# Performance work log

Measured on AMD Instinct MI355X. Metric: run time of the kernel, lower is better.

## Reference

```python
import math
import jax, jax.numpy as jnp
import numpy as np

H, N, L, B = 768, 64, 2048, 4
DT_MIN, DT_MAX = 1e-3, 1e-1


def setup_inputs() -> dict:
    key = jax.random.key(0)
    ks = jax.random.split(key, 7)
    # s4d_lin eigenvalue init: Re(lambda) = -0.5, Im(lambda) = pi*n
    log_neg_real = jnp.full((H, N), math.log(0.5), dtype=jnp.float32)
    imag = math.pi * jnp.broadcast_to(jnp.arange(N, dtype=jnp.float32)[None, :], (H, N))
    B_re = jax.random.normal(ks[0], (H, N), dtype=jnp.float32) * 0.5
    B_im = jax.random.normal(ks[1], (H, N), dtype=jnp.float32) * 0.5
    C_re = jax.random.normal(ks[2], (H, N), dtype=jnp.float32) * 0.5
    C_im = jax.random.normal(ks[3], (H, N), dtype=jnp.float32) * 0.5
    log_dt = jax.random.uniform(ks[4], (H,), dtype=jnp.float32) * (math.log(DT_MAX) - math.log(DT_MIN)) + math.log(DT_MIN)
    D = jax.random.normal(ks[5], (H,), dtype=jnp.float32) * 0.01
    u = jax.random.normal(ks[6], (B, H, L), dtype=jnp.float32)
    return {"u": u, "log_neg_real": log_neg_real, "imag": imag,
            "B_re": B_re, "B_im": B_im, "C_re": C_re, "C_im": C_im,
            "log_dt": log_dt, "D": D}


def reference(u, log_neg_real, imag, B_re, B_im, C_re, C_im, log_dt, D):
    Lseq = u.shape[-1]
    # eigenvalues with guaranteed Re < 0
    Lambda = -jnp.exp(log_neg_real) + 1j * imag              # (H, N) complex
    dt = jnp.exp(log_dt)[:, None]                            # (H, 1)
    # ZOH discretization
    A_bar = jnp.exp(Lambda * dt)                             # (H, N)
    B_bar = (A_bar - 1.0) * (1.0 / Lambda) * (B_re + 1j * B_im)
    C = C_re + 1j * C_im
    # Vandermonde kernel: K[h, l] = Re( sum_n C*B_bar * A_bar^l )
    powers = jnp.arange(Lseq, dtype=jnp.float32)             # (L,)
    A_powers = jnp.exp(jnp.log(A_bar)[:, :, None] * powers[None, None, :])  # (H, N, L)
    K = jnp.sum((C * B_bar)[:, :, None] * A_powers, axis=1).real            # (H, L)
    # causal conv via FFT with 2L zero-padding
    fft_len = 2 * Lseq
    u_f = jnp.fft.rfft(u, n=fft_len, axis=-1)                # (B, H, fft/2+1)
    K_f = jnp.fft.rfft(K, n=fft_len, axis=-1)                # (H, fft/2+1)
    y = jnp.fft.irfft(u_f * K_f[None], n=fft_len, axis=-1)[..., :Lseq]
    return y + D[None, :, None] * u
```

## Files before the change

kernel.cpp:

```cpp
#include <hip/hip_runtime.h>

#define HH 768
#define NN 64
#define LL 2048
#define BB 4

#define UF_OFF 0
#define WB_OFF 8704
#define SZ_OFF 26112
#define KP_OFF 43008
#define AB_OFF 43520
#define CB_OFF 44032
#define POOL_SZ 44544

__device__ __forceinline__ float2 cmul(float2 a, float2 b) {
    return make_float2(fmaf(a.x, b.x, -(a.y * b.y)), fmaf(a.x, b.y, a.y * b.x));
}
__device__ __forceinline__ float2 cfma(float2 a, float2 b, float2 acc) {
    acc.x = fmaf(a.x, b.x, fmaf(-a.y, b.y, acc.x));
    acc.y = fmaf(a.x, b.y, fmaf(a.y, b.x, acc.y));
    return acc;
}
__device__ __forceinline__ float2 astep(float2 A, float2 s, float uu) {
    return make_float2(fmaf(A.x, s.x, fmaf(-A.y, s.y, uu)),
                       fmaf(A.x, s.y, A.y * s.x));
}
__device__ __forceinline__ unsigned short f2bf(float x) {
    union { float f; unsigned u; } v; v.f = x;
    return (unsigned short)((v.u + 0x7fffu + ((v.u >> 16) & 1u)) >> 16);
}
__device__ __forceinline__ float lo2f(unsigned v) {
    union { unsigned u; float f; } x; x.u = v << 16; return x.f;
}
__device__ __forceinline__ float hi2f(unsigned v) {
    union { unsigned u; float f; } x; x.u = v & 0xffff0000u; return x.f;
}

__global__ __launch_bounds__(256, 3) void ssm_kernel6(
    const float* __restrict__ ug,
    const float* __restrict__ lnr,
    const float* __restrict__ img,
    const float* __restrict__ Brp,
    const float* __restrict__ Bip,
    const float* __restrict__ Crp,
    const float* __restrict__ Cip,
    const float* __restrict__ ldt,
    const float* __restrict__ Dp,
    float* __restrict__ outg)
{
    __shared__ __align__(16) unsigned char POOL[POOL_SZ];
    float*        UF   = (float*)(POOL + UF_OFF);
    unsigned int* WB   = (unsigned int*)(POOL + WB_OFF);
    float*        SZ   = (float*)(POOL + SZ_OFF);
    float*        kpad = (float*)(POOL + KP_OFF);
    float2*       Abar = (float2*)(POOL + AB_OFF);
    float2*       CBb  = (float2*)(POOL + CB_OFF);

    const int tid = threadIdx.x;
    const int h = blockIdx.x % HH;
    const int b = blockIdx.x / HH;
    const int lane = tid & 63;
    const int w = tid >> 6;

    const float dt = expf(ldt[h]);
    const float Dh = Dp[h];

    if (tid < NN) {
        const int n = tid;
        const float lre = -expf(lnr[h * NN + n]);
        const float lim = img[h * NN + n];
        const float e = expf(lre * dt);
        const float th = lim * dt;
        const float2 A = make_float2(e * cosf(th), e * sinf(th));
        const float den = lre * lre + lim * lim;
        const float2 invL = make_float2(lre / den, -lim / den);
        const float2 am1 = make_float2(A.x - 1.0f, A.y);
        const float2 Bb = cmul(cmul(am1, invL), make_float2(Brp[h*NN+n], Bip[h*NN+n]));
        const float2 CB = cmul(make_float2(Crp[h*NN+n], Cip[h*NN+n]), Bb);
        Abar[n] = A;
        CBb[n] = CB;
        kpad[n] = 0.f;
    }
    {
        const float4* u4g = (const float4*)(ug + (size_t)(b * HH + h) * LL);
        float4* uf4 = (float4*)UF;
        #pragma unroll
        for (int r = 0; r < 2; ++r) {
            const int i = tid + 256 * r;
            uf4[(i >> 4) * 17 + (i & 15)] = u4g[i];
        }
    }
    __syncthreads();

    {
        const float2 A = Abar[lane];
        const float2 a2 = cmul(A, A), a4 = cmul(a2, a2), a8 = cmul(a4, a4), a16 = cmul(a8, a8);
        float2 pw = cmul(CBb[lane], A);
        for (int i = 0; i < w; ++i) pw = cmul(pw, a16);
        #pragma unroll
        for (int jj = 0; jj < 16; ++jj) {
            const int j = 16 * w + jj;
            WB[lane * 68 + j] = (unsigned)f2bf(pw.x) | ((unsigned)f2bf(pw.y) << 16);
            SZ[j * 66 + lane] = pw.x;
            pw = cmul(pw, A);
        }
    }
    __syncthreads();

    if (w == 0) {
        float acc = 0.f;
        if (lane == 0) {
            for (int n = 0; n < NN; ++n) acc += CBb[n].x;
        } else {
            const float* row = &SZ[(lane - 1) * 66];
            #pragma unroll 8
            for (int n = 0; n < NN; ++n) acc += row[n];
        }
        kpad[64 + lane] = acc;
    }
    float2 Sres[8];
    {
        const float2 A = Abar[lane];
        const float2 p2 = cmul(A, A), p4 = cmul(p2, p2), p8 = cmul(p4, p4);
        float2 P8[8];
        P8[0] = make_float2(1.f, 0.f);
        #pragma unroll
        for (int k = 1; k < 8; ++k) P8[k] = cmul(P8[k-1], p8);
        const float4* uf4 = (const float4*)UF;
        #pragma unroll
        for (int k8 = 0; k8 < 8; ++k8) {
            const int c = w + 4 * k8;
            float2 sg[8];
            #pragma unroll
            for (int g = 0; g < 8; ++g) {
                const float4 ua = uf4[c * 17 + 2 * g];
                const float4 ub = uf4[c * 17 + 2 * g + 1];
                float2 s = make_float2(ua.x, 0.f);
                s = astep(A, s, ua.y);
                s = astep(A, s, ua.z);
                s = astep(A, s, ua.w);
                s = astep(A, s, ub.x);
                s = astep(A, s, ub.y);
                s = astep(A, s, ub.z);
                s = astep(A, s, ub.w);
                sg[g] = s;
            }
            float2 S = sg[7];
            #pragma unroll
            for (int g = 0; g < 7; ++g) S = cfma(P8[7 - g], sg[g], S);
            Sres[k8] = S;
        }
    }
    __syncthreads();

    #pragma unroll
    for (int k8 = 0; k8 < 8; ++k8) {
        const int c = w + 4 * k8;
        SZ[c * 132 + lane]      = Sres[k8].x;
        SZ[c * 132 + 64 + lane] = Sres[k8].y;
    }
    __syncthreads();

    if (w == 0) {
        const float2 A = Abar[lane];
        const float2 a2 = cmul(A, A), a4 = cmul(a2, a2), a8 = cmul(a4, a4),
                     a16 = cmul(a8, a8), a32 = cmul(a16, a16), a64 = cmul(a32, a32);
        float xr = 0.f, xi = 0.f;
        for (int c = 0; c < 32; ++c) {
            const float sr = SZ[c * 132 + lane];
            const float si = SZ[c * 132 + 64 + lane];
            SZ[c * 132 + lane]      = xr;
            SZ[c * 132 + 64 + lane] = xi;
            const float nxr = fmaf(a64.x, xr, fmaf(-a64.y, xi, sr));
            xi = fmaf(a64.x, xi, fmaf(a64.y, xr, si));
            xr = nxr;
        }
    }
    const int jt = tid & 15;
    const int ct = tid >> 4;
    const int c0 = ct, c1 = ct + 16;
    float a00 = 0.f, a01 = 0.f, a02 = 0.f, a03 = 0.f;
    float a10 = 0.f, a11 = 0.f, a12 = 0.f, a13 = 0.f;
    {
        const float4* u4 = (const float4*)UF;
        const float4* kp4 = (const float4*)kpad;
        #pragma unroll 4
        for (int s4 = 0; s4 < 16; ++s4) {
            const float4 ua = u4[c0 * 17 + s4];
            const float4 ub = u4[c1 * 17 + s4];
            const float4 Av = kp4[15 + jt - s4];
            const float4 Bv = kp4[16 + jt - s4];
            a00 = fmaf(Bv.x, ua.x, a00); a01 = fmaf(Bv.y, ua.x, a01);
            a02 = fmaf(Bv.z, ua.x, a02); a03 = fmaf(Bv.w, ua.x, a03);
            a10 = fmaf(Bv.x, ub.x, a10); a11 = fmaf(Bv.y, ub.x, a11);
            a12 = fmaf(Bv.z, ub.x, a12); a13 = fmaf(Bv.w, ub.x, a13);
            a00 = fmaf(Av.w, ua.y, a00); a01 = fmaf(Bv.x, ua.y, a01);
            a02 = fmaf(Bv.y, ua.y, a02); a03 = fmaf(Bv.z, ua.y, a03);
            a10 = fmaf(Av.w, ub.y, a10); a11 = fmaf(Bv.x, ub.y, a11);
            a12 = fmaf(Bv.y, ub.y, a12); a13 = fmaf(Bv.z, ub.y, a13);
            a00 = fmaf(Av.z, ua.z, a00); a01 = fmaf(Av.w, ua.z, a01);
            a02 = fmaf(Bv.x, ua.z, a02); a03 = fmaf(Bv.y, ua.z, a03);
            a10 = fmaf(Av.z, ub.z, a10); a11 = fmaf(Av.w, ub.z, a11);
            a12 = fmaf(Bv.x, ub.z, a12); a13 = fmaf(Bv.y, ub.z, a13);
            a00 = fmaf(Av.y, ua.w, a00); a01 = fmaf(Av.z, ua.w, a01);
            a02 = fmaf(Av.w, ua.w, a02); a03 = fmaf(Bv.x, ua.w, a03);
            a10 = fmaf(Av.y, ub.w, a10); a11 = fmaf(Av.z, ub.w, a11);
            a12 = fmaf(Av.w, ub.w, a12); a13 = fmaf(Bv.x, ub.w, a13);
        }
    }
    __syncthreads();

    {
        #pragma unroll 8
        for (int n = 0; n < NN; ++n) {
            const uint4 wp = *(const uint4*)&WB[n * 68 + 4 * jt];
            const float xr0 = SZ[c0 * 132 + n], xi0 = SZ[c0 * 132 + 64 + n];
            const float xr1 = SZ[c1 * 132 + n], xi1 = SZ[c1 * 132 + 64 + n];
            const float wr0 = lo2f(wp.x), wi0 = hi2f(wp.x);
            const float wr1 = lo2f(wp.y), wi1 = hi2f(wp.y);
            const float wr2 = lo2f(wp.z), wi2 = hi2f(wp.z);
            const float wr3 = lo2f(wp.w), wi3 = hi2f(wp.w);
            a00 = fmaf(wr0, xr0, fmaf(-wi0, xi0, a00));
            a01 = fmaf(wr1, xr0, fmaf(-wi1, xi0, a01));
            a02 = fmaf(wr2, xr0, fmaf(-wi2, xi0, a02));
            a03 = fmaf(wr3, xr0, fmaf(-wi3, xi0, a03));
            a10 = fmaf(wr0, xr1, fmaf(-wi0, xi1, a10));
            a11 = fmaf(wr1, xr1, fmaf(-wi1, xi1, a11));
            a12 = fmaf(wr2, xr1, fmaf(-wi2, xi1, a12));
            a13 = fmaf(wr3, xr1, fmaf(-wi3, xi1, a13));
        }
    }
    {
        const float4* u4 = (const float4*)UF;
        const float4 uA = u4[c0 * 17 + jt];
        const float4 uB = u4[c1 * 17 + jt];
        float4* o4 = (float4*)(outg + (size_t)(b * HH + h) * LL);
        o4[c0 * 16 + jt] = make_float4(fmaf(Dh, uA.x, a00), fmaf(Dh, uA.y, a01),
                                       fmaf(Dh, uA.z, a02), fmaf(Dh, uA.w, a03));
        o4[c1 * 16 + jt] = make_float4(fmaf(Dh, uB.x, a10), fmaf(Dh, uB.y, a11),
                                       fmaf(Dh, uB.z, a12), fmaf(Dh, uB.w, a13));
    }
}

extern "C" void kernel_launch(void* const* d_in, const int* in_sizes, int n_in,
                              void* d_out, int out_size, void* d_ws, size_t ws_size,
                              hipStream_t stream) {
    (void)in_sizes; (void)n_in; (void)out_size; (void)d_ws; (void)ws_size;
    ssm_kernel6<<<dim3(BB * HH), dim3(256), 0, stream>>>(
        (const float*)d_in[0], (const float*)d_in[1], (const float*)d_in[2],
        (const float*)d_in[3], (const float*)d_in[4], (const float*)d_in[5],
        (const float*)d_in[6], (const float*)d_in[7], (const float*)d_in[8],
        (float*)d_out);
}
```

Measured before the change: 163.5 us.

## Use packed FP32 FMAs, fp32 real weights, and skip masked causal conv work

The chunk scan, chunk combine and the chunk-to-output projection now use packed two-wide FP32 FMA vectors. The 8-step recurrence is rewritten as precomputed powers A1..A4 applied across two 4-element halves. The weight table splits into an fp32 real part and a bf16-packed imaginary part, and the kernel-tap sum reads the real table directly so the extra SZ copy goes away. The thread-to-output mapping changes so each wave owns a fixed range of in-chunk positions, which lets the short direct convolution loop stop at its causal bound instead of always running 16 steps. One barrier before the SZ write is also removed. In exchange, LDS use grows, which may lower occupancy, the wave loop bounds now differ, and the dropped barrier risks a race between SZ writes and the earlier WRE reads.

```diff
diff --git a/kernel.cpp b/kernel.cpp
--- a/kernel.cpp
+++ b/kernel.cpp
@@ -5,25 +5,19 @@
 #define LL 2048
 #define BB 4
 
-#define UF_OFF 0
-#define WB_OFF 8704
-#define SZ_OFF 26112
-#define KP_OFF 43008
-#define AB_OFF 43520
-#define CB_OFF 44032
-#define POOL_SZ 44544
+typedef __attribute__((ext_vector_type(2))) float f32x2;
+
+#define UF_OFF  0
+#define WRE_OFF 8704
+#define WIM_OFF 26112
+#define SZ_OFF  34560
+#define KP_OFF  51200
+#define AB_OFF  51712
+#define CB_OFF  52224
+#define POOL_SZ 52736
 
 __device__ __forceinline__ float2 cmul(float2 a, float2 b) {
     return make_float2(fmaf(a.x, b.x, -(a.y * b.y)), fmaf(a.x, b.y, a.y * b.x));
-}
-__device__ __forceinline__ float2 cfma(float2 a, float2 b, float2 acc) {
-    acc.x = fmaf(a.x, b.x, fmaf(-a.y, b.y, acc.x));
-    acc.y = fmaf(a.x, b.y, fmaf(a.y, b.x, acc.y));
-    return acc;
-}
-__device__ __forceinline__ float2 astep(float2 A, float2 s, float uu) {
-    return make_float2(fmaf(A.x, s.x, fmaf(-A.y, s.y, uu)),
-                       fmaf(A.x, s.y, A.y * s.x));
 }
 __device__ __forceinline__ unsigned short f2bf(float x) {
     union { float f; unsigned u; } v; v.f = x;
@@ -35,8 +29,16 @@
 __device__ __forceinline__ float hi2f(unsigned v) {
     union { unsigned u; float f; } x; x.u = v & 0xffff0000u; return x.f;
 }
-
-__global__ __launch_bounds__(256, 3) void ssm_kernel6(
+__device__ __forceinline__ f32x2 pkfma(f32x2 a, f32x2 b, f32x2 c) {
+    return __builtin_elementwise_fma(a, b, c);
+}
+__device__ __forceinline__ f32x2 splat2(float x) { return (f32x2){x, x}; }
+__device__ __forceinline__ f32x2 swapneg(f32x2 v) { return (f32x2){-v[1], v[0]}; }
+__device__ __forceinline__ f32x2 cmul2(f32x2 a, f32x2 b) {
+    return pkfma(splat2(a[0]), b, splat2(a[1]) * swapneg(b));
+}
+
+__global__ __launch_bounds__(256, 3) void ssm_kernel7(
     const float* __restrict__ ug,
     const float* __restrict__ lnr,
     const float* __restrict__ img,
@@ -50,7 +52,8 @@
 {
     __shared__ __align__(16) unsigned char POOL[POOL_SZ];
     float*        UF   = (float*)(POOL + UF_OFF);
-    unsigned int* WB   = (unsigned int*)(POOL + WB_OFF);
+    float*        WRE  = (float*)(POOL + WRE_OFF);
+    unsigned int* WIM  = (unsigned int*)(POOL + WIM_OFF);
     float*        SZ   = (float*)(POOL + SZ_OFF);
     float*        kpad = (float*)(POOL + KP_OFF);
     float2*       Abar = (float2*)(POOL + AB_OFF);
@@ -97,11 +100,13 @@
         const float2 a2 = cmul(A, A), a4 = cmul(a2, a2), a8 = cmul(a4, a4), a16 = cmul(a8, a8);
         float2 pw = cmul(CBb[lane], A);
         for (int i = 0; i < w; ++i) pw = cmul(pw, a16);
+        unsigned prevlo = 0;
         #pragma unroll
         for (int jj = 0; jj < 16; ++jj) {
             const int j = 16 * w + jj;
-            WB[lane * 68 + j] = (unsigned)f2bf(pw.x) | ((unsigned)f2bf(pw.y) << 16);
-            SZ[j * 66 + lane] = pw.x;
+            WRE[lane * 68 + j] = pw.x;
+            if ((jj & 1) == 0) prevlo = (unsigned)f2bf(pw.y);
+            else WIM[lane * 33 + (j >> 1)] = prevlo | ((unsigned)f2bf(pw.y) << 16);
             pw = cmul(pw, A);
         }
     }
@@ -112,52 +117,55 @@
         if (lane == 0) {
             for (int n = 0; n < NN; ++n) acc += CBb[n].x;
         } else {
-            const float* row = &SZ[(lane - 1) * 66];
+            const float* col = WRE + (lane - 1);
             #pragma unroll 8
-            for (int n = 0; n < NN; ++n) acc += row[n];
+            for (int n = 0; n < NN; ++n) acc += col[n * 68];
         }
         kpad[64 + lane] = acc;
     }
-    float2 Sres[8];
-    {
-        const float2 A = Abar[lane];
-        const float2 p2 = cmul(A, A), p4 = cmul(p2, p2), p8 = cmul(p4, p4);
-        float2 P8[8];
-        P8[0] = make_float2(1.f, 0.f);
-        #pragma unroll
-        for (int k = 1; k < 8; ++k) P8[k] = cmul(P8[k-1], p8);
+    f32x2 Sres[8];
+    {
+        const float2 Af = Abar[lane];
+        const f32x2 A1 = {Af.x, Af.y};
+        const f32x2 A2 = cmul2(A1, A1);
+        const f32x2 A3 = cmul2(A2, A1);
+        const f32x2 A4 = cmul2(A2, A2);
+        const f32x2 A8 = cmul2(A4, A4);
+        f32x2 P8[8];
+        P8[0] = (f32x2){1.f, 0.f};
+        #pragma unroll
+        for (int k = 1; k < 8; ++k) P8[k] = cmul2(P8[k-1], A8);
         const float4* uf4 = (const float4*)UF;
         #pragma unroll
         for (int k8 = 0; k8 < 8; ++k8) {
             const int c = w + 4 * k8;
-            float2 sg[8];
+            f32x2 sg[8];
             #pragma unroll
             for (int g = 0; g < 8; ++g) {
                 const float4 ua = uf4[c * 17 + 2 * g];
                 const float4 ub = uf4[c * 17 + 2 * g + 1];
-                float2 s = make_float2(ua.x, 0.f);
-                s = astep(A, s, ua.y);
-                s = astep(A, s, ua.z);
-                s = astep(A, s, ua.w);
-                s = astep(A, s, ub.x);
-                s = astep(A, s, ub.y);
-                s = astep(A, s, ub.z);
-                s = astep(A, s, ub.w);
-                sg[g] = s;
+                f32x2 t = A3 * ua.x;
+                t = pkfma(A2, splat2(ua.y), t);
+                t = pkfma(A1, splat2(ua.z), t);
+                t[0] += ua.w;
+                f32x2 t2 = A3 * ub.x;
+                t2 = pkfma(A2, splat2(ub.y), t2);
+                t2 = pkfma(A1, splat2(ub.z), t2);
+                t2[0] += ub.w;
+                sg[g] = pkfma(splat2(A4[0]), t, pkfma(splat2(A4[1]), swapneg(t), t2));
             }
-            float2 S = sg[7];
+            f32x2 S = sg[7];
             #pragma unroll
-            for (int g = 0; g < 7; ++g) S = cfma(P8[7 - g], sg[g], S);
+            for (int g = 0; g < 7; ++g)
+                S = pkfma(splat2(P8[7-g][0]), sg[g], pkfma(splat2(P8[7-g][1]), swapneg(sg[g]), S));
             Sres[k8] = S;
         }
     }
-    __syncthreads();
-
     #pragma unroll
     for (int k8 = 0; k8 < 8; ++k8) {
         const int c = w + 4 * k8;
-        SZ[c * 132 + lane]      = Sres[k8].x;
-        SZ[c * 132 + 64 + lane] = Sres[k8].y;
+        SZ[c * 130 + lane]      = Sres[k8][0];
+        SZ[c * 130 + 64 + lane] = Sres[k8][1];
     }
     __syncthreads();
 
@@ -167,25 +175,27 @@
                      a16 = cmul(a8, a8), a32 = cmul(a16, a16), a64 = cmul(a32, a32);
         float xr = 0.f, xi = 0.f;
         for (int c = 0; c < 32; ++c) {
-            const float sr = SZ[c * 132 + lane];
-            const float si = SZ[c * 132 + 64 + lane];
-            SZ[c * 132 + lane]      = xr;
-            SZ[c * 132 + 64 + lane] = xi;
+            const float sr = SZ[c * 130 + lane];
+            const float si = SZ[c * 130 + 64 + lane];
+            SZ[c * 130 + lane]      = xr;
+            SZ[c * 130 + 64 + lane] = xi;
             const float nxr = fmaf(a64.x, xr, fmaf(-a64.y, xi, sr));
             xi = fmaf(a64.x, xi, fmaf(a64.y, xr, si));
             xr = nxr;
         }
     }
-    const int jt = tid & 15;
-    const int ct = tid >> 4;
-    const int c0 = ct, c1 = ct + 16;
+    const int jl = lane & 3;
+    const int jt = 4 * w + jl;
+    const int c0 = lane >> 2;
+    const int c1 = c0 + 16;
     float a00 = 0.f, a01 = 0.f, a02 = 0.f, a03 = 0.f;
     float a10 = 0.f, a11 = 0.f, a12 = 0.f, a13 = 0.f;
     {
         const float4* u4 = (const float4*)UF;
         const float4* kp4 = (const float4*)kpad;
+        const int smax = 4 * w + 4;
         #pragma unroll 4
-        for (int s4 = 0; s4 < 16; ++s4) {
+        for (int s4 = 0; s4 < smax; ++s4) {
             const float4 ua = u4[c0 * 17 + s4];
             const float4 ub = u4[c1 * 17 + s4];
             const float4 Av = kp4[15 + jt - s4];
@@ -211,34 +221,39 @@
     __syncthreads();
 
     {
-        #pragma unroll 8
+        const int j0 = 4 * jt;
+        f32x2 r01 = {a00, a01}, r23 = {a02, a03};
+        f32x2 s01 = {a10, a11}, s23 = {a12, a13};
+        #pragma unroll 4
         for (int n = 0; n < NN; ++n) {
-            const uint4 wp = *(const uint4*)&WB[n * 68 + 4 * jt];
-            const float xr0 = SZ[c0 * 132 + n], xi0 = SZ[c0 * 132 + 64 + n];
-            const float xr1 = SZ[c1 * 132 + n], xi1 = SZ[c1 * 132 + 64 + n];
-            const float wr0 = lo2f(wp.x), wi0 = hi2f(wp.x);
-            const float wr1 = lo2f(wp.y), wi1 = hi2f(wp.y);
-            const float wr2 = lo2f(wp.z), wi2 = hi2f(wp.z);
-            const float wr3 = lo2f(wp.w), wi3 = hi2f(wp.w);
-            a00 = fmaf(wr0, xr0, fmaf(-wi0, xi0, a00));
-            a01 = fmaf(wr1, xr0, fmaf(-wi1, xi0, a01));
-            a02 = fmaf(wr2, xr0, fmaf(-wi2, xi0, a02));
-            a03 = fmaf(wr3, xr0, fmaf(-wi3, xi0, a03));
-            a10 = fmaf(wr0, xr1, fmaf(-wi0, xi1, a10));
-            a11 = fmaf(wr1, xr1, fmaf(-wi1, xi1, a11));
-            a12 = fmaf(wr2, xr1, fmaf(-wi2, xi1, a12));
-            a13 = fmaf(wr3, xr1, fmaf(-wi3, xi1, a13));
-        }
-    }
-    {
+            const float4 wr = *(const float4*)&WRE[n * 68 + j0];
+            const unsigned wa = WIM[n * 33 + (j0 >> 1)];
+            const unsigned wb = WIM[n * 33 + (j0 >> 1) + 1];
+            const float xr0 = SZ[c0 * 130 + n], xi0 = SZ[c0 * 130 + 64 + n];
+            const float xr1 = SZ[c1 * 130 + n], xi1 = SZ[c1 * 130 + 64 + n];
+            const f32x2 wr01 = {wr.x, wr.y}, wr23 = {wr.z, wr.w};
+            const f32x2 wi01 = {lo2f(wa), hi2f(wa)};
+            const f32x2 wi23 = {lo2f(wb), hi2f(wb)};
+            r01 = pkfma(wr01, splat2(xr0), r01);
+            r23 = pkfma(wr23, splat2(xr0), r23);
+            s01 = pkfma(wr01, splat2(xr1), s01);
+            s23 = pkfma(wr23, splat2(xr1), s23);
+            const float nxi0 = -xi0, nxi1 = -xi1;
+            r01 = pkfma(wi01, splat2(nxi0), r01);
+            r23 = pkfma(wi23, splat2(nxi0), r23);
+            s01 = pkfma(wi01, splat2(nxi1), s01);
+            s23 = pkfma(wi23, splat2(nxi1), s23);
+        }
         const float4* u4 = (const float4*)UF;
         const float4 uA = u4[c0 * 17 + jt];
         const float4 uB = u4[c1 * 17 + jt];
-        float4* o4 = (float4*)(outg + (size_t)(b * HH + h) * LL);
-        o4[c0 * 16 + jt] = make_float4(fmaf(Dh, uA.x, a00), fmaf(Dh, uA.y, a01),
-                                       fmaf(Dh, uA.z, a02), fmaf(Dh, uA.w, a03));
-        o4[c1 * 16 + jt] = make_float4(fmaf(Dh, uB.x, a10), fmaf(Dh, uB.y, a11),
-                                       fmaf(Dh, uB.z, a12), fmaf(Dh, uB.w, a13));
+        float* og = outg + (size_t)(b * HH + h) * LL;
+        *(float4*)(og + (size_t)c0 * 64 + j0) =
+            make_float4(fmaf(Dh, uA.x, r01[0]), fmaf(Dh, uA.y, r01[1]),
+                        fmaf(Dh, uA.z, r23[0]), fmaf(Dh, uA.w, r23[1]));
+        *(float4*)(og + (size_t)c1 * 64 + j0) =
+            make_float4(fmaf(Dh, uB.x, s01[0]), fmaf(Dh, uB.y, s01[1]),
+                        fmaf(Dh, uB.z, s23[0]), fmaf(Dh, uB.w, s23[1]));
     }
 }
 
@@ -246,7 +261,7 @@
                               void* d_out, int out_size, void* d_ws, size_t ws_size,
                               hipStream_t stream) {
     (void)in_sizes; (void)n_in; (void)out_size; (void)d_ws; (void)ws_size;
-    ssm_kernel6<<<dim3(BB * HH), dim3(256), 0, stream>>>(
+    ssm_kernel7<<<dim3(BB * HH), dim3(256), 0, stream>>>(
         (const float*)d_in[0], (const float*)d_in[1], (const float*)d_in[2],
         (const float*)d_in[3], (const float*)d_in[4], (const float*)d_in[5],
         (const float*)d_in[6], (const float*)d_in[7], (const float*)d_in[8],
```

New measurement: 152.2 us. 1.07x faster.
